# Optimization experiments

Measured on AMD Instinct MI355X. Metric: run time of the kernel, lower is better.

Reference implementation:

```python
import jax, jax.numpy as jnp
import numpy as np

N = 4096
NFEAT = 1024
NHID = 512
NCLS = 32
NLAYERS = 3
SPARSITY = 0.002


def _l2norm(x, eps=1e-12):
    n = jnp.sqrt(jnp.sum(x * x, axis=1, keepdims=True))
    return x / jnp.maximum(n, eps)


def setup_inputs() -> dict:
    key = jax.random.key(0)
    ks = jax.random.split(key, 12)
    # sparse-valued dense adjacency (original stores torch.sparse but densifies every hop)
    vals = jax.random.uniform(ks[0], (N, N), dtype=jnp.float32)
    mask = jax.random.uniform(ks[1], (N, N)) < SPARSITY
    adj = jnp.where(mask, vals, 0.0)
    features = jax.random.normal(ks[2], (N, NFEAT), dtype=jnp.float32)
    # y is a one-hot label matrix [N, nclass]
    labels = jax.random.randint(ks[3], (N,), 0, NCLS)
    y = jax.nn.one_hot(labels, NCLS, dtype=jnp.float32)
    s = 0.02
    W0 = jax.random.normal(ks[4], (NFEAT + 3 * NCLS, NHID), dtype=jnp.float32) * s
    b0 = jnp.zeros((NHID,), jnp.float32)
    W1_0 = jax.random.normal(ks[5], (NHID + 3 * NCLS, NHID), dtype=jnp.float32) * s
    b1_0 = jnp.zeros((NHID,), jnp.float32)
    W1_1 = jax.random.normal(ks[6], (NHID + 3 * NCLS, NHID), dtype=jnp.float32) * s
    b1_1 = jnp.zeros((NHID,), jnp.float32)
    W2 = jax.random.normal(ks[7], (NFEAT + NHID, NCLS), dtype=jnp.float32) * s
    b2 = jnp.zeros((NCLS,), jnp.float32)
    alphas = jnp.ones((NLAYERS, 5), jnp.float32)
    return {
        "adj": adj, "features": features, "y": y,
        "W0": W0, "b0": b0, "W1_0": W1_0, "b1_0": b1_0,
        "W1_1": W1_1, "b1_1": b1_1, "W2": W2, "b2": b2,
        "alphas": alphas, "layer_norm": 1,
    }


def reference(adj, features, y, W0, b0, W1_0, b1_0, W1_1, b1_1, W2, b2, alphas, layer_norm):
    Ws = [(W0, b0), (W1_0, b1_0), (W1_1, b1_1)]
    initial_features = jax.lax.stop_gradient(features)  # .clone().detach()
    feats = features
    max_features = None
    pow_adj = adj  # persists across layers (faithful to original): hops adj, adj^2, adj^4
    for i in range(NLAYERS):
        mask_alpha = jax.nn.softmax(alphas[i], axis=0)
        for _ in range(i):
            pow_adj = adj @ pow_adj
        hop = pow_adj @ feats                                   # [N, d]
        dist = (pow_adj > 0).astype(adj.dtype)                  # binarized reachability
        y_out = dist @ y                                        # [N, c]
        y_in = dist.T @ y                                       # [N, c]
        y_all = y_in + y_out
        hop = mask_alpha[0] * hop
        y_out = mask_alpha[1] * y_out
        y_in = mask_alpha[2] * y_in
        y_all = mask_alpha[3] * y_all
        mat = jnp.concatenate([hop, y_out, y_in, y_all], axis=1)
        W, b = Ws[i]
        tmp = mat @ W + b
        if layer_norm:
            tmp = _l2norm(tmp)
        feats = tmp
        max_features = tmp if max_features is None else jnp.maximum(max_features, tmp)
    final_mat = jnp.concatenate([initial_features, max_features], axis=1)
    out = jax.nn.relu(final_mat)
    # dropout: eval mode (identity)
    out = out @ W2 + b2
    return jax.nn.log_softmax(out, axis=1)
```

## Files before the change

### kernel.cpp

```cpp
#include <hip/hip_runtime.h>
#include <hip/hip_bf16.h>
#include <math.h>

typedef unsigned long long u64;
typedef unsigned short ushort_t;
typedef float f32x4 __attribute__((ext_vector_type(4)));
typedef short s16x8 __attribute__((ext_vector_type(8)));

#define NN 4096
#define NF 1024
#define NH 512
#define NC 32
#define LDP 40
#define K0 (NF + 3*NC)
#define K1 (NH + 3*NC)

__device__ inline float bf2f(ushort_t u) {
    unsigned int v = ((unsigned int)u) << 16;
    return __uint_as_float(v);
}
__device__ inline ushort_t f2bf(float f) {
    __hip_bfloat16 h = __float2bfloat16(f);
    return *(ushort_t*)&h;
}

__device__ void role_build(int i, int l, const float* __restrict__ adj,
                           u64* __restrict__ B1, int* __restrict__ rowcnt,
                           int* __restrict__ colidx, float* __restrict__ vals) {
    const float* row = adj + (size_t)i * NN + l * 64;
    const float4* row4 = (const float4*)row;
    u64 w = 0;
    #pragma unroll
    for (int k = 0; k < 16; ++k) {
        float4 v = row4[k];
        if (v.x > 0.f) w |= 1ULL << (4*k + 0);
        if (v.y > 0.f) w |= 1ULL << (4*k + 1);
        if (v.z > 0.f) w |= 1ULL << (4*k + 2);
        if (v.w > 0.f) w |= 1ULL << (4*k + 3);
    }
    B1[(size_t)i*64 + l] = w;
    int cnt = __popcll(w);
    int pre = cnt;
    #pragma unroll
    for (int o = 1; o < 64; o <<= 1) {
        int u = __shfl_up(pre, o, 64);
        if (l >= o) pre += u;
    }
    int excl = pre - cnt;
    int total = __shfl(pre, 63, 64);
    u64 ww = w;
    int idx = excl;
    while (ww) {
        int b = __ffsll((unsigned long long)ww) - 1;
        ww &= ww - 1;
        if (idx < 64) {
            colidx[i*64 + idx] = l*64 + b;
            vals[i*64 + idx] = row[b];
        }
        ++idx;
    }
    int tot = total < 64 ? total : 64;
    for (int s = tot + l; s < 64; s += 64) {
        colidx[i*64 + s] = 0;
        vals[i*64 + s] = 0.f;
    }
    if (l == 0) rowcnt[i] = (tot + 3) & ~3;
}

__global__ __launch_bounds__(256) void k_setup(const float* __restrict__ adj,
        const float* __restrict__ features, __hip_bfloat16* __restrict__ featb,
        const float* __restrict__ y, u64* __restrict__ LC,
        const float* __restrict__ W0, const float* __restrict__ W1_0,
        const float* __restrict__ W1_1,
        __hip_bfloat16* __restrict__ Wt0, __hip_bfloat16* __restrict__ Wt1,
        __hip_bfloat16* __restrict__ Wt2,
        const float* __restrict__ alphas, float* __restrict__ a_sm,
        u64* __restrict__ B1, int* __restrict__ rowcnt,
        int* __restrict__ colidx, float* __restrict__ vals) {
    __shared__ __align__(16) char smem[4352];
    int b = blockIdx.x;
    int t = threadIdx.x;
    int wid = t >> 6, l = t & 63;
    if (b < 1024) {
        role_build(b*4 + wid, l, adj, B1, rowcnt, colidx, vals);
    } else if (b < 5120) {
        int base = (b - 1024) * 1024 + t * 4;
        float4 v = *(const float4*)&features[base];
        ushort4 o;
        o.x = f2bf(v.x); o.y = f2bf(v.y); o.z = f2bf(v.z); o.w = f2bf(v.w);
        *(ushort4*)&((ushort_t*)featb)[base] = o;
    } else if (b < 5136) {
        int w = (b - 5120) * 4 + wid;
        const float* yr = y + (size_t)(w*64 + l) * NC;
        for (int c = 0; c < NC; ++c) {
            u64 m = __ballot(yr[c] > 0.5f);
            if (l == c) LC[c*64 + w] = m;
        }
    } else if (b < 6304) {
        const float* W; __hip_bfloat16* Wt; int K, ktiles, idx;
        if (b < 5696)      { W = W0;   Wt = Wt0; K = K0; ktiles = 35; idx = b - 5136; }
        else if (b < 6000) { W = W1_0; Wt = Wt1; K = K1; ktiles = 19; idx = b - 5696; }
        else               { W = W1_1; Wt = Wt2; K = K1; ktiles = 19; idx = b - 6000; }
        float (*tile)[33] = (float(*)[33])smem;
        int kb = (idx % ktiles) * 32, nb = (idx / ktiles) * 32;
        int tc = t & 31, tr8 = t >> 5;
        for (int r = tr8; r < 32; r += 8)
            tile[r][tc] = W[(size_t)(kb + r) * NH + nb + tc];
        __syncthreads();
        ushort_t* Wu = (ushort_t*)Wt;
        for (int r = tr8; r < 32; r += 8)
            Wu[(size_t)(nb + r) * K + kb + tc] = f2bf(tile[tc][r]);
    } else {
        if (t == 0) {
            for (int i = 0; i < 3; ++i) {
                float m = -1e30f;
                for (int j = 0; j < 5; ++j) m = fmaxf(m, alphas[i*5+j]);
                float e[5]; float s = 0.f;
                for (int j = 0; j < 5; ++j) { e[j] = expf(alphas[i*5+j] - m); s += e[j]; }
                for (int j = 0; j < 5; ++j) a_sm[i*5+j] = e[j] / s;
            }
        }
    }
}

__device__ void role_bsq(int i, int t, char* smem, const u64* __restrict__ Bidx,
                         const u64* __restrict__ Bdat, u64* __restrict__ Bout) {
    u64* ridx = (u64*)smem;
    u64* part = ridx + 64;
    int wid = t >> 6, lane = t & 63;
    if (t < 64) ridx[t] = Bidx[(size_t)i*64 + t];
    __syncthreads();
    u64 acc = 0;
    for (int u = wid*16; u < wid*16 + 16; ++u) {
        u64 w = ridx[u];
        while (w) {
            int k = u*64 + (__ffsll((unsigned long long)w) - 1);
            w &= (w - 1);
            acc |= Bdat[(size_t)k*64 + lane];
        }
    }
    part[wid*64 + lane] = acc;
    __syncthreads();
    if (t < 64) Bout[(size_t)i*64 + t] = part[t] | part[64+t] | part[128+t] | part[192+t];
}

__device__ void role_btrans(int tb, int wid, int l, char* smem,
                            const u64* __restrict__ B, u64* __restrict__ BT) {
    u64* ld = ((u64*)smem) + wid*64;
    int I = tb >> 6, J = tb & 63;
    ld[l] = B[(size_t)(I*64 + l)*64 + J];
    __syncthreads();
    u64 out = 0;
    #pragma unroll
    for (int r = 0; r < 64; ++r) out |= ((ld[r] >> l) & 1ULL) << r;
    BT[(size_t)(J*64 + l)*64 + I] = out;
}

__device__ void role_ymat(int rb, int t, char* smem, const u64* __restrict__ B,
                          const u64* __restrict__ BT, const u64* __restrict__ LC,
                          const float* __restrict__ asp, ushort_t* __restrict__ m,
                          int d, int K) {
    u64* LCt   = (u64*)smem;
    u64* rows  = LCt + 64*32;
    u64* rowsT = rows + 8*64;
    for (int k = t; k < 2048; k += 256) {
        int c = k >> 6, w = k & 63;
        LCt[w*32 + c] = LC[k];
    }
    for (int k = t; k < 512; k += 256) {
        int r = k >> 6, w = k & 63;
        rows[r*64 + w]  = B[(size_t)(rb + r)*64 + w];
        rowsT[r*64 + w] = BT[(size_t)(rb + r)*64 + w];
    }
    __syncthreads();
    int wid = t >> 6, lane = t & 63;
    int h = lane >> 5, c = lane & 31;
    int r = wid * 2 + h;
    int co = 0, ci = 0;
    #pragma unroll
    for (int w = 0; w < 64; ++w) {
        u64 lc = LCt[w*32 + c];
        co += __popcll(rows[r*64 + w]  & lc);
        ci += __popcll(rowsT[r*64 + w] & lc);
    }
    float a1 = asp[1], a2 = asp[2], a3 = asp[3];
    size_t i = rb + r;
    m[i*K + d + c]      = f2bf(a1 * (float)co);
    m[i*K + d + 32 + c] = f2bf(a2 * (float)ci);
    m[i*K + d + 64 + c] = f2bf(a3 * (float)(co + ci));
}

__device__ void role_spmm_bf(int i, int tx, const int* __restrict__ rc,
                             const int* __restrict__ ci, const float* __restrict__ vl,
                             const ushort_t* __restrict__ X, int d,
                             ushort_t* __restrict__ Y, int ystride, float alpha) {
    int cnt = rc[i];
    float acc[8] = {0,0,0,0,0,0,0,0};
    for (int p = 0; p < cnt; p += 4) {
        int4   cc = *(const int4*)&ci[(size_t)i*64 + p];
        float4 vv = *(const float4*)&vl[(size_t)i*64 + p];
        s16x8 x0 = *(const s16x8*)&X[(size_t)cc.x * d + 8*tx];
        s16x8 x1 = *(const s16x8*)&X[(size_t)cc.y * d + 8*tx];
        s16x8 x2 = *(const s16x8*)&X[(size_t)cc.z * d + 8*tx];
        s16x8 x3 = *(const s16x8*)&X[(size_t)cc.w * d + 8*tx];
        #pragma unroll
        for (int j = 0; j < 8; ++j) {
            acc[j] += vv.x * bf2f((ushort_t)x0[j]);
            acc[j] += vv.y * bf2f((ushort_t)x1[j]);
            acc[j] += vv.z * bf2f((ushort_t)x2[j]);
            acc[j] += vv.w * bf2f((ushort_t)x3[j]);
        }
    }
    s16x8 o;
    #pragma unroll
    for (int j = 0; j < 8; ++j) o[j] = (short)f2bf(alpha * acc[j]);
    *(s16x8*)&Y[(size_t)i*ystride + 8*tx] = o;
}

__device__ void role_spmm_f32s(int i, int tx, const int* __restrict__ rc,
                               const int* __restrict__ ci, const float* __restrict__ vl,
                               const float* __restrict__ src, const float* __restrict__ parts,
                               int ln, ushort_t* __restrict__ Y, int ystride, float alpha) {
    int cnt = rc[i];
    float acc[8] = {0,0,0,0,0,0,0,0};
    for (int p = 0; p < cnt; p += 4) {
        int4   cc = *(const int4*)&ci[(size_t)i*64 + p];
        float4 vv = *(const float4*)&vl[(size_t)i*64 + p];
        int cols[4] = {cc.x, cc.y, cc.z, cc.w};
        float vs4[4] = {vv.x, vv.y, vv.z, vv.w};
        #pragma unroll
        for (int e = 0; e < 4; ++e) {
            int col = cols[e];
            float4 pa = *(const float4*)&parts[col*8];
            float4 pb = *(const float4*)&parts[col*8 + 4];
            float ss = pa.x+pa.y+pa.z+pa.w + pb.x+pb.y+pb.z+pb.w;
            float sc = ln ? 1.0f / fmaxf(sqrtf(ss), 1e-12f) : 1.0f;
            float vsc = vs4[e] * sc;
            float4 xa = *(const float4*)&src[(size_t)col*NH + 8*tx];
            float4 xb = *(const float4*)&src[(size_t)col*NH + 8*tx + 4];
            acc[0] += vsc*xa.x; acc[1] += vsc*xa.y; acc[2] += vsc*xa.z; acc[3] += vsc*xa.w;
            acc[4] += vsc*xb.x; acc[5] += vsc*xb.y; acc[6] += vsc*xb.z; acc[7] += vsc*xb.w;
        }
    }
    s16x8 o;
    #pragma unroll
    for (int j = 0; j < 8; ++j) o[j] = (short)f2bf(alpha * acc[j]);
    *(s16x8*)&Y[(size_t)i*ystride + 8*tx] = o;
}

__device__ void role_gemm(int bx, int tid, char* smem,
                          const ushort_t* __restrict__ mat, const ushort_t* __restrict__ Wt,
                          const float* __restrict__ bias, float* __restrict__ C,
                          float* __restrict__ parts, int K) {
    ushort_t* As = (ushort_t*)smem;
    ushort_t* Bs = As + 64*LDP;
    int xcd = bx & 7, rest = bx >> 3;
    int nt = rest & 7, mt = (rest >> 3) * 8 + xcd;
    int bm = mt * 64, bn = nt * 64;
    int srow = tid >> 2, scol = (tid & 3) * 8;
    int wid = tid >> 6, lane = tid & 63;
    int fr = lane & 15, hi2 = lane >> 4, fk = hi2 * 8;
    f32x4 acc[4] = {{0,0,0,0},{0,0,0,0},{0,0,0,0},{0,0,0,0}};
    const ushort_t* Au = mat + (size_t)(bm + srow) * K + scol;
    const ushort_t* Bu = Wt  + (size_t)(bn + srow) * K + scol;
    for (int k0 = 0; k0 < K; k0 += 32) {
        *(s16x8*)&As[srow * LDP + scol] = *(const s16x8*)(Au + k0);
        *(s16x8*)&Bs[srow * LDP + scol] = *(const s16x8*)(Bu + k0);
        __syncthreads();
        s16x8 af = *(const s16x8*)&As[(wid * 16 + fr) * LDP + fk];
        #pragma unroll
        for (int j = 0; j < 4; ++j) {
            s16x8 bfv = *(const s16x8*)&Bs[(j * 16 + fr) * LDP + fk];
            acc[j] = __builtin_amdgcn_mfma_f32_16x16x32_bf16(af, bfv, acc[j], 0, 0, 0);
        }
        __syncthreads();
    }
    int drow = bm + wid * 16 + hi2 * 4;
    #pragma unroll
    for (int r = 0; r < 4; ++r) {
        float ps = 0.f;
        #pragma unroll
        for (int j = 0; j < 4; ++j) {
            float v = acc[j][r] + bias[bn + j*16 + fr];
            ps += v * v;
        }
        #pragma unroll
        for (int o = 1; o < 16; o <<= 1) ps += __shfl_xor(ps, o, 64);
        if (fr == 0) parts[(size_t)(drow + r) * 8 + nt] = ps;
    }
    #pragma unroll
    for (int j = 0; j < 4; ++j) {
        int col = bn + j * 16 + fr;
        float bv = bias[col];
        #pragma unroll
        for (int r = 0; r < 4; ++r)
            C[(size_t)(drow + r) * NH + col] = acc[j][r] + bv;
    }
}

__global__ __launch_bounds__(256) void k_phase2(const int* __restrict__ rowcnt,
        const int* __restrict__ colidx, const float* __restrict__ vals,
        const __hip_bfloat16* __restrict__ featb, __hip_bfloat16* __restrict__ mat0,
        const float* __restrict__ a_sm,
        const u64* __restrict__ B1, u64* __restrict__ B2, u64* __restrict__ B1T) {
    __shared__ __align__(16) char smem[2560];
    int b = blockIdx.x;
    int t = threadIdx.x;
    int wid = t >> 6, l = t & 63;
    if (b < 2048) {
        role_spmm_bf(b*2 + (t >> 7), t & 127, rowcnt, colidx, vals,
                     (const ushort_t*)featb, NF, (ushort_t*)mat0, K0, a_sm[0]);
    } else if (b < 6144) {
        role_bsq(b - 2048, t, smem, B1, B1, B2);
    } else {
        role_btrans((b - 6144)*4 + wid, wid, l, smem, B1, B1T);
    }
}

__global__ __launch_bounds__(256) void k_phase3(const u64* __restrict__ B1,
        const u64* __restrict__ B2, u64* __restrict__ B3, u64* __restrict__ B2T,
        const u64* __restrict__ B1T, const u64* __restrict__ LC,
        const float* __restrict__ a_sm, __hip_bfloat16* __restrict__ mat0) {
    __shared__ __align__(16) char smem[24576];
    int b = blockIdx.x;
    int t = threadIdx.x;
    int wid = t >> 6, l = t & 63;
    if (b < 4096) {
        role_bsq(b, t, smem, B1, B2, B3);
    } else if (b < 5120) {
        role_btrans((b - 4096)*4 + wid, wid, l, smem, B2, B2T);
    } else {
        role_ymat((b - 5120)*8, t, smem, B1, B1T, LC, a_sm, (ushort_t*)mat0, NF, K0);
    }
}

__global__ __launch_bounds__(256) void k_phase4(const __hip_bfloat16* __restrict__ mat0,
        const __hip_bfloat16* __restrict__ Wt0, const float* __restrict__ b0,
        float* __restrict__ tmp0, float* __restrict__ parts0,
        const u64* __restrict__ B1, const u64* __restrict__ B3, u64* __restrict__ B4,
        const u64* __restrict__ B2, const u64* __restrict__ B2T,
        const u64* __restrict__ LC, const float* __restrict__ a_sm,
        __hip_bfloat16* __restrict__ mat1) {
    __shared__ __align__(16) char smem[24576];
    int b = blockIdx.x;
    int t = threadIdx.x;
    if (b < 512) {
        role_gemm(b, t, smem, (const ushort_t*)mat0, (const ushort_t*)Wt0, b0,
                  tmp0, parts0, K0);
    } else if (b < 4608) {
        role_bsq(b - 512, t, smem, B1, B3, B4);
    } else {
        role_ymat((b - 4608)*8, t, smem, B2, B2T, LC, a_sm + 5, (ushort_t*)mat1, NH, K1);
    }
}

__global__ __launch_bounds__(256) void k_phase5(const u64* __restrict__ B4,
        u64* __restrict__ B4T,
        const int* __restrict__ rowcnt, const int* __restrict__ colidx,
        const float* __restrict__ vals, const float* __restrict__ tmp0,
        const float* __restrict__ parts0, const int* __restrict__ lnflag,
        __hip_bfloat16* __restrict__ u1) {
    __shared__ __align__(16) char smem[2048];
    int b = blockIdx.x;
    int t = threadIdx.x;
    int wid = t >> 6, l = t & 63;
    if (b < 1024) {
        role_btrans(b*4 + wid, wid, l, smem, B4, B4T);
    } else {
        role_spmm_f32s((b - 1024)*4 + wid, l, rowcnt, colidx, vals, tmp0, parts0,
                       *lnflag, (ushort_t*)u1, NH, 1.0f);
    }
}

__global__ __launch_bounds__(256) void k_phase6(const int* __restrict__ rowcnt,
        const int* __restrict__ colidx, const float* __restrict__ vals,
        const __hip_bfloat16* __restrict__ u1, __hip_bfloat16* __restrict__ mat1,
        const float* __restrict__ a_sm,
        const u64* __restrict__ B4, const u64* __restrict__ B4T,
        const u64* __restrict__ LC, __hip_bfloat16* __restrict__ mat2) {
    __shared__ __align__(16) char smem[24576];
    int b = blockIdx.x;
    int t = threadIdx.x;
    if (b < 1024) {
        role_spmm_bf(b*4 + (t >> 6), t & 63, rowcnt, colidx, vals,
                     (const ushort_t*)u1, NH, (ushort_t*)mat1, K1, a_sm[5]);
    } else {
        role_ymat((b - 1024)*8, t, smem, B4, B4T, LC, a_sm + 10, (ushort_t*)mat2, NH, K1);
    }
}

__global__ __launch_bounds__(256) void k_gemm(const __hip_bfloat16* __restrict__ mat,
        const __hip_bfloat16* __restrict__ Wt, const float* __restrict__ bias,
        float* __restrict__ C, float* __restrict__ parts, int K) {
    __shared__ __align__(16) char smem[2 * 64 * LDP * 2];
    role_gemm(blockIdx.x, threadIdx.x, smem, (const ushort_t*)mat, (const ushort_t*)Wt,
              bias, C, parts, K);
}

__global__ __launch_bounds__(256) void k_spmm_f(const int* __restrict__ rc,
        const int* __restrict__ ci, const float* __restrict__ vl,
        const float* __restrict__ src, const float* __restrict__ parts,
        const int* __restrict__ lnflag, __hip_bfloat16* __restrict__ Y,
        int ystride) {
    role_spmm_f32s(blockIdx.x*4 + (threadIdx.x >> 6), threadIdx.x & 63, rc, ci, vl,
                   src, parts, *lnflag, (ushort_t*)Y, ystride, 1.0f);
}

__global__ __launch_bounds__(256) void k_spmm_b(const int* __restrict__ rc,
        const int* __restrict__ ci, const float* __restrict__ vl,
        const __hip_bfloat16* __restrict__ X, __hip_bfloat16* __restrict__ Y,
        int ystride, const float* __restrict__ a_sm, int ai) {
    float alpha = (ai >= 0) ? a_sm[ai] : 1.0f;
    role_spmm_bf(blockIdx.x*4 + (threadIdx.x >> 6), threadIdx.x & 63, rc, ci, vl,
                 (const ushort_t*)X, NH, (ushort_t*)Y, ystride, alpha);
}

__global__ __launch_bounds__(256) void k_l2final(const float* __restrict__ tmp0,
        const float* __restrict__ parts0, const float* __restrict__ tmp1,
        const float* __restrict__ parts1, const float* __restrict__ tmp2,
        const float* __restrict__ parts2, const float* __restrict__ feat0,
        const float* __restrict__ W2, const float* __restrict__ b2,
        const int* __restrict__ lnflag, float* __restrict__ out) {
    int rb = blockIdx.x * 8;
    int t = threadIdx.x;
    __shared__ float rows[8][NF + NH];
    __shared__ float part[8][8][32];
    for (int r = 0; r < 8; ++r) {
        const float* f0 = feat0 + (size_t)(rb + r) * NF;
        for (int c = t; c < NF; c += 256) rows[r][c] = fmaxf(f0[c], 0.f);
    }
    int wid = t >> 6, lane = t & 63;
    int ln = *lnflag;
    #pragma unroll
    for (int rr = 0; rr < 2; ++rr) {
        int r = wid * 2 + rr;
        int row = rb + r;
        float s0, s1, s2;
        {
            float4 a0 = *(const float4*)&parts0[row*8], b0v = *(const float4*)&parts0[row*8+4];
            float4 a1 = *(const float4*)&parts1[row*8], b1v = *(const float4*)&parts1[row*8+4];
            float4 a2 = *(const float4*)&parts2[row*8], b2v = *(const float4*)&parts2[row*8+4];
            float q0 = a0.x+a0.y+a0.z+a0.w + b0v.x+b0v.y+b0v.z+b0v.w;
            float q1 = a1.x+a1.y+a1.z+a1.w + b1v.x+b1v.y+b1v.z+b1v.w;
            float q2 = a2.x+a2.y+a2.z+a2.w + b2v.x+b2v.y+b2v.z+b2v.w;
            s0 = ln ? 1.0f / fmaxf(sqrtf(q0), 1e-12f) : 1.0f;
            s1 = ln ? 1.0f / fmaxf(sqrtf(q1), 1e-12f) : 1.0f;
            s2 = ln ? 1.0f / fmaxf(sqrtf(q2), 1e-12f) : 1.0f;
        }
        const float4* t0 = (const float4*)(tmp0 + (size_t)row * NH + lane * 8);
        const float4* t1 = (const float4*)(tmp1 + (size_t)row * NH + lane * 8);
        const float4* t2 = (const float4*)(tmp2 + (size_t)row * NH + lane * 8);
        float* dst = &rows[r][NF + lane * 8];
        #pragma unroll
        for (int h = 0; h < 2; ++h) {
            float4 v0 = t0[h], v1 = t1[h], v2 = t2[h];
            dst[h*4+0] = fmaxf(fmaxf(fmaxf(v0.x*s0, v1.x*s1), v2.x*s2), 0.f);
            dst[h*4+1] = fmaxf(fmaxf(fmaxf(v0.y*s0, v1.y*s1), v2.y*s2), 0.f);
            dst[h*4+2] = fmaxf(fmaxf(fmaxf(v0.z*s0, v1.z*s1), v2.z*s2), 0.f);
            dst[h*4+3] = fmaxf(fmaxf(fmaxf(v0.w*s0, v1.w*s1), v2.w*s2), 0.f);
        }
    }
    __syncthreads();
    int c = t & 31, g = t >> 5;
    float acc[8] = {0,0,0,0,0,0,0,0};
    for (int k = g * 192; k < (g + 1) * 192; ++k) {
        float w = W2[(size_t)k * NC + c];
        #pragma unroll
        for (int r = 0; r < 8; ++r) acc[r] += rows[r][k] * w;
    }
    #pragma unroll
    for (int r = 0; r < 8; ++r) part[g][r][c] = acc[r];
    __syncthreads();
    int r = g;
    float lg = b2[c];
    #pragma unroll
    for (int gg = 0; gg < 8; ++gg) lg += part[gg][r][c];
    float m = lg;
    #pragma unroll
    for (int o = 16; o > 0; o >>= 1) m = fmaxf(m, __shfl_xor(m, o, 32));
    float e = expf(lg - m), s = e;
    #pragma unroll
    for (int o = 16; o > 0; o >>= 1) s += __shfl_xor(s, o, 32);
    out[(size_t)(rb + r) * NC + c] = lg - m - logf(s);
}

extern "C" void kernel_launch(void* const* d_in, const int* in_sizes, int n_in,
                              void* d_out, int out_size, void* d_ws, size_t ws_size,
                              hipStream_t stream) {
    const float* adj      = (const float*)d_in[0];
    const float* features = (const float*)d_in[1];
    const float* y        = (const float*)d_in[2];
    const float* W0       = (const float*)d_in[3];
    const float* b0       = (const float*)d_in[4];
    const float* W1_0     = (const float*)d_in[5];
    const float* b1_0     = (const float*)d_in[6];
    const float* W1_1     = (const float*)d_in[7];
    const float* b1_1     = (const float*)d_in[8];
    const float* W2       = (const float*)d_in[9];
    const float* b2       = (const float*)d_in[10];
    const float* alphas   = (const float*)d_in[11];
    const int*   lnflag   = (const int*)d_in[12];
    float* out = (float*)d_out;

    char* ws = (char*)d_ws;
    size_t off = 0;
    auto alloc = [&](size_t bytes) -> char* {
        char* p = ws + off;
        off = (off + bytes + 255) & ~(size_t)255;
        return p;
    };
    float* a_sm   = (float*)alloc(16 * 4);
    int*   rowcnt = (int*)alloc((size_t)NN * 4);
    int*   colidx = (int*)alloc((size_t)NN * 64 * 4);
    float* vals   = (float*)alloc((size_t)NN * 64 * 4);
    u64* B1  = (u64*)alloc((size_t)NN * 64 * 8);
    u64* B2  = (u64*)alloc((size_t)NN * 64 * 8);
    u64* B3  = (u64*)alloc((size_t)NN * 64 * 8);
    u64* B4  = (u64*)alloc((size_t)NN * 64 * 8);
    u64* B1T = (u64*)alloc((size_t)NN * 64 * 8);
    u64* B2T = (u64*)alloc((size_t)NN * 64 * 8);
    u64* B4T = (u64*)alloc((size_t)NN * 64 * 8);
    u64* LC  = (u64*)alloc((size_t)NC * 64 * 8);
    __hip_bfloat16* featb = (__hip_bfloat16*)alloc((size_t)NN * NF * 2);
    __hip_bfloat16* t1b   = (__hip_bfloat16*)alloc((size_t)NN * NH * 2);
    __hip_bfloat16* t2b   = (__hip_bfloat16*)alloc((size_t)NN * NH * 2);
    __hip_bfloat16* mat0  = (__hip_bfloat16*)alloc((size_t)NN * K0 * 2);
    __hip_bfloat16* mat1  = (__hip_bfloat16*)alloc((size_t)NN * K1 * 2);
    __hip_bfloat16* mat2  = (__hip_bfloat16*)alloc((size_t)NN * K1 * 2);
    __hip_bfloat16* Wt0   = (__hip_bfloat16*)alloc((size_t)NH * K0 * 2);
    __hip_bfloat16* Wt1   = (__hip_bfloat16*)alloc((size_t)NH * K1 * 2);
    __hip_bfloat16* Wt2   = (__hip_bfloat16*)alloc((size_t)NH * K1 * 2);
    float* tmp0   = (float*)alloc((size_t)NN * NH * 4);
    float* tmp1   = (float*)alloc((size_t)NN * NH * 4);
    float* tmp2   = (float*)alloc((size_t)NN * NH * 4);
    float* parts0 = (float*)alloc((size_t)NN * 8 * 4);
    float* parts1 = (float*)alloc((size_t)NN * 8 * 4);
    float* parts2 = (float*)alloc((size_t)NN * 8 * 4);

    k_setup<<<6305, 256, 0, stream>>>(adj, features, featb, y, LC, W0, W1_0, W1_1,
                                      Wt0, Wt1, Wt2, alphas, a_sm,
                                      B1, rowcnt, colidx, vals);
    k_phase2<<<7168, 256, 0, stream>>>(rowcnt, colidx, vals, featb, mat0, a_sm,
                                       B1, B2, B1T);
    k_phase3<<<5632, 256, 0, stream>>>(B1, B2, B3, B2T, B1T, LC, a_sm, mat0);
    k_phase4<<<5120, 256, 0, stream>>>(mat0, Wt0, b0, tmp0, parts0,
                                       B1, B3, B4, B2, B2T, LC, a_sm, mat1);
    k_phase5<<<2048, 256, 0, stream>>>(B4, B4T, rowcnt, colidx, vals,
                                       tmp0, parts0, lnflag, t1b);
    k_phase6<<<1536, 256, 0, stream>>>(rowcnt, colidx, vals, t1b, mat1, a_sm,
                                       B4, B4T, LC, mat2);
    k_gemm<<<512, 256, 0, stream>>>(mat1, Wt1, b1_0, tmp1, parts1, K1);
    k_spmm_f<<<NN/4, 256, 0, stream>>>(rowcnt, colidx, vals, tmp1, parts1, lnflag, t1b, NH);
    k_spmm_b<<<NN/4, 256, 0, stream>>>(rowcnt, colidx, vals, t1b, t2b, NH, a_sm, -1);
    k_spmm_b<<<NN/4, 256, 0, stream>>>(rowcnt, colidx, vals, t2b, t1b, NH, a_sm, -1);
    k_spmm_b<<<NN/4, 256, 0, stream>>>(rowcnt, colidx, vals, t1b, mat2, K1, a_sm, 10);
    k_gemm<<<512, 256, 0, stream>>>(mat2, Wt2, b1_1, tmp2, parts2, K1);
    k_l2final<<<NN/8, 256, 0, stream>>>(tmp0, parts0, tmp1, parts1, tmp2, parts2,
                                        features, W2, b2, lnflag, out);
}
```

Before: 215.5 us.

## Reassociate hops: multiply features by weights before sparse propagation, split label-count GEMM

After: 236.8 us. 9.9% more time.

```diff
diff --git a/kernel.cpp b/kernel.cpp
--- a/kernel.cpp
+++ b/kernel.cpp
@@ -12,8 +12,6 @@
 #define NH 512
 #define NC 32
 #define LDP 40
-#define K0 (NF + 3*NC)
-#define K1 (NH + 3*NC)
 
 __device__ inline float bf2f(ushort_t u) {
     unsigned int v = ((unsigned int)u) << 16;
@@ -64,63 +62,23 @@
         colidx[i*64 + s] = 0;
         vals[i*64 + s] = 0.f;
     }
-    if (l == 0) rowcnt[i] = (tot + 3) & ~3;
-}
-
-__global__ __launch_bounds__(256) void k_setup(const float* __restrict__ adj,
-        const float* __restrict__ features, __hip_bfloat16* __restrict__ featb,
-        const float* __restrict__ y, u64* __restrict__ LC,
-        const float* __restrict__ W0, const float* __restrict__ W1_0,
-        const float* __restrict__ W1_1,
-        __hip_bfloat16* __restrict__ Wt0, __hip_bfloat16* __restrict__ Wt1,
-        __hip_bfloat16* __restrict__ Wt2,
-        const float* __restrict__ alphas, float* __restrict__ a_sm,
-        u64* __restrict__ B1, int* __restrict__ rowcnt,
-        int* __restrict__ colidx, float* __restrict__ vals) {
-    __shared__ __align__(16) char smem[4352];
-    int b = blockIdx.x;
-    int t = threadIdx.x;
-    int wid = t >> 6, l = t & 63;
-    if (b < 1024) {
-        role_build(b*4 + wid, l, adj, B1, rowcnt, colidx, vals);
-    } else if (b < 5120) {
-        int base = (b - 1024) * 1024 + t * 4;
-        float4 v = *(const float4*)&features[base];
-        ushort4 o;
-        o.x = f2bf(v.x); o.y = f2bf(v.y); o.z = f2bf(v.z); o.w = f2bf(v.w);
-        *(ushort4*)&((ushort_t*)featb)[base] = o;
-    } else if (b < 5136) {
-        int w = (b - 5120) * 4 + wid;
-        const float* yr = y + (size_t)(w*64 + l) * NC;
-        for (int c = 0; c < NC; ++c) {
-            u64 m = __ballot(yr[c] > 0.5f);
-            if (l == c) LC[c*64 + w] = m;
-        }
-    } else if (b < 6304) {
-        const float* W; __hip_bfloat16* Wt; int K, ktiles, idx;
-        if (b < 5696)      { W = W0;   Wt = Wt0; K = K0; ktiles = 35; idx = b - 5136; }
-        else if (b < 6000) { W = W1_0; Wt = Wt1; K = K1; ktiles = 19; idx = b - 5696; }
-        else               { W = W1_1; Wt = Wt2; K = K1; ktiles = 19; idx = b - 6000; }
-        float (*tile)[33] = (float(*)[33])smem;
-        int kb = (idx % ktiles) * 32, nb = (idx / ktiles) * 32;
-        int tc = t & 31, tr8 = t >> 5;
-        for (int r = tr8; r < 32; r += 8)
-            tile[r][tc] = W[(size_t)(kb + r) * NH + nb + tc];
-        __syncthreads();
-        ushort_t* Wu = (ushort_t*)Wt;
-        for (int r = tr8; r < 32; r += 8)
-            Wu[(size_t)(nb + r) * K + kb + tc] = f2bf(tile[tc][r]);
-    } else {
-        if (t == 0) {
-            for (int i = 0; i < 3; ++i) {
-                float m = -1e30f;
-                for (int j = 0; j < 5; ++j) m = fmaxf(m, alphas[i*5+j]);
-                float e[5]; float s = 0.f;
-                for (int j = 0; j < 5; ++j) { e[j] = expf(alphas[i*5+j] - m); s += e[j]; }
-                for (int j = 0; j < 5; ++j) a_sm[i*5+j] = e[j] / s;
-            }
-        }
-    }
+    if (l == 0) {
+        int r8 = (tot + 7) & ~7;
+        rowcnt[i] = r8 < 64 ? r8 : 64;
+    }
+}
+
+__device__ void role_wt(const float* __restrict__ W, ushort_t* __restrict__ Wt,
+                        int ksrc0, int Kd, int idx, char* smem, int t) {
+    float (*tile)[33] = (float(*)[33])smem;
+    int ktiles = Kd >> 5;
+    int kb = (idx % ktiles) * 32, nb = (idx / ktiles) * 32;
+    int tc = t & 31, tr8 = t >> 5;
+    for (int r = tr8; r < 32; r += 8)
+        tile[r][tc] = W[(size_t)(ksrc0 + kb + r) * NH + nb + tc];
+    __syncthreads();
+    for (int r = tr8; r < 32; r += 8)
+        Wt[(size_t)(nb + r) * Kd + kb + tc] = f2bf(tile[tc][r]);
 }
 
 __device__ void role_bsq(int i, int t, char* smem, const u64* __restrict__ Bidx,
@@ -158,8 +116,7 @@
 
 __device__ void role_ymat(int rb, int t, char* smem, const u64* __restrict__ B,
                           const u64* __restrict__ BT, const u64* __restrict__ LC,
-                          const float* __restrict__ asp, ushort_t* __restrict__ m,
-                          int d, int K) {
+                          const float* __restrict__ asp, ushort_t* __restrict__ yc) {
     u64* LCt   = (u64*)smem;
     u64* rows  = LCt + 64*32;
     u64* rowsT = rows + 8*64;
@@ -185,73 +142,15 @@
     }
     float a1 = asp[1], a2 = asp[2], a3 = asp[3];
     size_t i = rb + r;
-    m[i*K + d + c]      = f2bf(a1 * (float)co);
-    m[i*K + d + 32 + c] = f2bf(a2 * (float)ci);
-    m[i*K + d + 64 + c] = f2bf(a3 * (float)(co + ci));
-}
-
-__device__ void role_spmm_bf(int i, int tx, const int* __restrict__ rc,
-                             const int* __restrict__ ci, const float* __restrict__ vl,
-                             const ushort_t* __restrict__ X, int d,
-                             ushort_t* __restrict__ Y, int ystride, float alpha) {
-    int cnt = rc[i];
-    float acc[8] = {0,0,0,0,0,0,0,0};
-    for (int p = 0; p < cnt; p += 4) {
-        int4   cc = *(const int4*)&ci[(size_t)i*64 + p];
-        float4 vv = *(const float4*)&vl[(size_t)i*64 + p];
-        s16x8 x0 = *(const s16x8*)&X[(size_t)cc.x * d + 8*tx];
-        s16x8 x1 = *(const s16x8*)&X[(size_t)cc.y * d + 8*tx];
-        s16x8 x2 = *(const s16x8*)&X[(size_t)cc.z * d + 8*tx];
-        s16x8 x3 = *(const s16x8*)&X[(size_t)cc.w * d + 8*tx];
-        #pragma unroll
-        for (int j = 0; j < 8; ++j) {
-            acc[j] += vv.x * bf2f((ushort_t)x0[j]);
-            acc[j] += vv.y * bf2f((ushort_t)x1[j]);
-            acc[j] += vv.z * bf2f((ushort_t)x2[j]);
-            acc[j] += vv.w * bf2f((ushort_t)x3[j]);
-        }
-    }
-    s16x8 o;
-    #pragma unroll
-    for (int j = 0; j < 8; ++j) o[j] = (short)f2bf(alpha * acc[j]);
-    *(s16x8*)&Y[(size_t)i*ystride + 8*tx] = o;
-}
-
-__device__ void role_spmm_f32s(int i, int tx, const int* __restrict__ rc,
-                               const int* __restrict__ ci, const float* __restrict__ vl,
-                               const float* __restrict__ src, const float* __restrict__ parts,
-                               int ln, ushort_t* __restrict__ Y, int ystride, float alpha) {
-    int cnt = rc[i];
-    float acc[8] = {0,0,0,0,0,0,0,0};
-    for (int p = 0; p < cnt; p += 4) {
-        int4   cc = *(const int4*)&ci[(size_t)i*64 + p];
-        float4 vv = *(const float4*)&vl[(size_t)i*64 + p];
-        int cols[4] = {cc.x, cc.y, cc.z, cc.w};
-        float vs4[4] = {vv.x, vv.y, vv.z, vv.w};
-        #pragma unroll
-        for (int e = 0; e < 4; ++e) {
-            int col = cols[e];
-            float4 pa = *(const float4*)&parts[col*8];
-            float4 pb = *(const float4*)&parts[col*8 + 4];
-            float ss = pa.x+pa.y+pa.z+pa.w + pb.x+pb.y+pb.z+pb.w;
-            float sc = ln ? 1.0f / fmaxf(sqrtf(ss), 1e-12f) : 1.0f;
-            float vsc = vs4[e] * sc;
-            float4 xa = *(const float4*)&src[(size_t)col*NH + 8*tx];
-            float4 xb = *(const float4*)&src[(size_t)col*NH + 8*tx + 4];
-            acc[0] += vsc*xa.x; acc[1] += vsc*xa.y; acc[2] += vsc*xa.z; acc[3] += vsc*xa.w;
-            acc[4] += vsc*xb.x; acc[5] += vsc*xb.y; acc[6] += vsc*xb.z; acc[7] += vsc*xb.w;
-        }
-    }
-    s16x8 o;
-    #pragma unroll
-    for (int j = 0; j < 8; ++j) o[j] = (short)f2bf(alpha * acc[j]);
-    *(s16x8*)&Y[(size_t)i*ystride + 8*tx] = o;
-}
-
-__device__ void role_gemm(int bx, int tid, char* smem,
-                          const ushort_t* __restrict__ mat, const ushort_t* __restrict__ Wt,
-                          const float* __restrict__ bias, float* __restrict__ C,
-                          float* __restrict__ parts, int K) {
+    yc[i*96 + c]      = f2bf(a1 * (float)co);
+    yc[i*96 + 32 + c] = f2bf(a2 * (float)ci);
+    yc[i*96 + 64 + c] = f2bf(a3 * (float)(co + ci));
+}
+
+__device__ void role_gemm(int bx, int tid, char* smem, const ushort_t* __restrict__ Abf,
+                          const float* __restrict__ Af, int Ka,
+                          const ushort_t* __restrict__ Bt, int K,
+                          ushort_t* __restrict__ Cb, float* __restrict__ Cf) {
     ushort_t* As = (ushort_t*)smem;
     ushort_t* Bs = As + 64*LDP;
     int xcd = bx & 7, rest = bx >> 3;
@@ -261,11 +160,23 @@
     int wid = tid >> 6, lane = tid & 63;
     int fr = lane & 15, hi2 = lane >> 4, fk = hi2 * 8;
     f32x4 acc[4] = {{0,0,0,0},{0,0,0,0},{0,0,0,0},{0,0,0,0}};
-    const ushort_t* Au = mat + (size_t)(bm + srow) * K + scol;
-    const ushort_t* Bu = Wt  + (size_t)(bn + srow) * K + scol;
     for (int k0 = 0; k0 < K; k0 += 32) {
-        *(s16x8*)&As[srow * LDP + scol] = *(const s16x8*)(Au + k0);
-        *(s16x8*)&Bs[srow * LDP + scol] = *(const s16x8*)(Bu + k0);
+        if (Abf) {
+            *(s16x8*)&As[srow * LDP + scol] =
+                *(const s16x8*)&Abf[(size_t)(bm + srow) * Ka + k0 + scol];
+        } else {
+            const float* ap = &Af[(size_t)(bm + srow) * Ka + k0 + scol];
+            float4 a0 = *(const float4*)ap;
+            float4 a1 = *(const float4*)(ap + 4);
+            s16x8 o;
+            o[0] = (short)f2bf(a0.x); o[1] = (short)f2bf(a0.y);
+            o[2] = (short)f2bf(a0.z); o[3] = (short)f2bf(a0.w);
+            o[4] = (short)f2bf(a1.x); o[5] = (short)f2bf(a1.y);
+            o[6] = (short)f2bf(a1.z); o[7] = (short)f2bf(a1.w);
+            *(s16x8*)&As[srow * LDP + scol] = o;
+        }
+        *(s16x8*)&Bs[srow * LDP + scol] =
+            *(const s16x8*)&Bt[(size_t)(bn + srow) * K + k0 + scol];
         __syncthreads();
         s16x8 af = *(const s16x8*)&As[(wid * 16 + fr) * LDP + fk];
         #pragma unroll
@@ -277,211 +188,303 @@
     }
     int drow = bm + wid * 16 + hi2 * 4;
     #pragma unroll
-    for (int r = 0; r < 4; ++r) {
-        float ps = 0.f;
-        #pragma unroll
-        for (int j = 0; j < 4; ++j) {
-            float v = acc[j][r] + bias[bn + j*16 + fr];
-            ps += v * v;
-        }
-        #pragma unroll
-        for (int o = 1; o < 16; o <<= 1) ps += __shfl_xor(ps, o, 64);
-        if (fr == 0) parts[(size_t)(drow + r) * 8 + nt] = ps;
-    }
-    #pragma unroll
     for (int j = 0; j < 4; ++j) {
         int col = bn + j * 16 + fr;
-        float bv = bias[col];
         #pragma unroll
-        for (int r = 0; r < 4; ++r)
-            C[(size_t)(drow + r) * NH + col] = acc[j][r] + bv;
-    }
-}
-
-__global__ __launch_bounds__(256) void k_phase2(const int* __restrict__ rowcnt,
-        const int* __restrict__ colidx, const float* __restrict__ vals,
-        const __hip_bfloat16* __restrict__ featb, __hip_bfloat16* __restrict__ mat0,
-        const float* __restrict__ a_sm,
-        const u64* __restrict__ B1, u64* __restrict__ B2, u64* __restrict__ B1T) {
-    __shared__ __align__(16) char smem[2560];
-    int b = blockIdx.x;
-    int t = threadIdx.x;
+        for (int r = 0; r < 4; ++r) {
+            if (Cb) Cb[(size_t)(drow + r) * NH + col] = f2bf(acc[j][r]);
+            else    Cf[(size_t)(drow + r) * NH + col] = acc[j][r];
+        }
+    }
+}
+
+__device__ void role_sfin(int blk, int t, const float* __restrict__ F,
+                          const float* __restrict__ W2, float* __restrict__ sl) {
+    int r = t >> 5, c = t & 31;
+    int row = blk * 8 + r;
+    const float* fr_ = F + (size_t)row * NF;
+    float acc = 0.f;
+    for (int k = 0; k < NF; k += 4) {
+        float4 fv = *(const float4*)&fr_[k];
+        acc += fmaxf(fv.x, 0.f) * W2[(size_t)(k+0)*NC + c];
+        acc += fmaxf(fv.y, 0.f) * W2[(size_t)(k+1)*NC + c];
+        acc += fmaxf(fv.z, 0.f) * W2[(size_t)(k+2)*NC + c];
+        acc += fmaxf(fv.w, 0.f) * W2[(size_t)(k+3)*NC + c];
+    }
+    sl[(size_t)row*NC + c] = acc;
+}
+
+__device__ void role_spmm(int i, int lane, const int* __restrict__ rc,
+                          const int* __restrict__ ci, const float* __restrict__ vl,
+                          const ushort_t* __restrict__ X, ushort_t* __restrict__ Y) {
+    int cnt = rc[i];
+    float acc[8] = {0,0,0,0,0,0,0,0};
+    for (int p = 0; p < cnt; p += 8) {
+        int4   c0 = *(const int4*)&ci[i*64 + p];
+        int4   c1 = *(const int4*)&ci[i*64 + p + 4];
+        float4 v0 = *(const float4*)&vl[i*64 + p];
+        float4 v1 = *(const float4*)&vl[i*64 + p + 4];
+        s16x8 x0 = *(const s16x8*)&X[(size_t)c0.x * NH + 8*lane];
+        s16x8 x1 = *(const s16x8*)&X[(size_t)c0.y * NH + 8*lane];
+        s16x8 x2 = *(const s16x8*)&X[(size_t)c0.z * NH + 8*lane];
+        s16x8 x3 = *(const s16x8*)&X[(size_t)c0.w * NH + 8*lane];
+        s16x8 x4 = *(const s16x8*)&X[(size_t)c1.x * NH + 8*lane];
+        s16x8 x5 = *(const s16x8*)&X[(size_t)c1.y * NH + 8*lane];
+        s16x8 x6 = *(const s16x8*)&X[(size_t)c1.z * NH + 8*lane];
+        s16x8 x7 = *(const s16x8*)&X[(size_t)c1.w * NH + 8*lane];
+        #pragma unroll
+        for (int j = 0; j < 8; ++j) {
+            acc[j] += v0.x * bf2f((ushort_t)x0[j]);
+            acc[j] += v0.y * bf2f((ushort_t)x1[j]);
+            acc[j] += v0.z * bf2f((ushort_t)x2[j]);
+            acc[j] += v0.w * bf2f((ushort_t)x3[j]);
+            acc[j] += v1.x * bf2f((ushort_t)x4[j]);
+            acc[j] += v1.y * bf2f((ushort_t)x5[j]);
+            acc[j] += v1.z * bf2f((ushort_t)x6[j]);
+            acc[j] += v1.w * bf2f((ushort_t)x7[j]);
+        }
+    }
+    s16x8 o;
+    #pragma unroll
+    for (int j = 0; j < 8; ++j) o[j] = (short)f2bf(acc[j]);
+    *(s16x8*)&Y[(size_t)i*NH + 8*lane] = o;
+}
+
+__device__ void role_spmmF(int i, int lane, const int* __restrict__ rc,
+                           const int* __restrict__ ci, const float* __restrict__ vl,
+                           const ushort_t* __restrict__ X, const float* __restrict__ yv,
+                           const float* __restrict__ bias, int ln, float alpha,
+                           ushort_t* __restrict__ F) {
+    int cnt = rc[i];
+    float acc[8] = {0,0,0,0,0,0,0,0};
+    for (int p = 0; p < cnt; p += 8) {
+        int4   c0 = *(const int4*)&ci[i*64 + p];
+        int4   c1 = *(const int4*)&ci[i*64 + p + 4];
+        float4 v0 = *(const float4*)&vl[i*64 + p];
+        float4 v1 = *(const float4*)&vl[i*64 + p + 4];
+        s16x8 x0 = *(const s16x8*)&X[(size_t)c0.x * NH + 8*lane];
+        s16x8 x1 = *(const s16x8*)&X[(size_t)c0.y * NH + 8*lane];
+        s16x8 x2 = *(const s16x8*)&X[(size_t)c0.z * NH + 8*lane];
+        s16x8 x3 = *(const s16x8*)&X[(size_t)c0.w * NH + 8*lane];
+        s16x8 x4 = *(const s16x8*)&X[(size_t)c1.x * NH + 8*lane];
+        s16x8 x5 = *(const s16x8*)&X[(size_t)c1.y * NH + 8*lane];
+        s16x8 x6 = *(const s16x8*)&X[(size_t)c1.z * NH + 8*lane];
+        s16x8 x7 = *(const s16x8*)&X[(size_t)c1.w * NH + 8*lane];
+        #pragma unroll
+        for (int j = 0; j < 8; ++j) {
+            acc[j] += v0.x * bf2f((ushort_t)x0[j]);
+            acc[j] += v0.y * bf2f((ushort_t)x1[j]);
+            acc[j] += v0.z * bf2f((ushort_t)x2[j]);
+            acc[j] += v0.w * bf2f((ushort_t)x3[j]);
+            acc[j] += v1.x * bf2f((ushort_t)x4[j]);
+            acc[j] += v1.y * bf2f((ushort_t)x5[j]);
+            acc[j] += v1.z * bf2f((ushort_t)x6[j]);
+            acc[j] += v1.w * bf2f((ushort_t)x7[j]);
+        }
+    }
+    const float* yr = yv + (size_t)i * NH + 8*lane;
+    float4 ya = *(const float4*)yr;
+    float4 yb = *(const float4*)(yr + 4);
+    float4 ba = *(const float4*)&bias[8*lane];
+    float4 bb = *(const float4*)&bias[8*lane + 4];
+    float v[8];
+    v[0] = alpha*acc[0] + ya.x + ba.x; v[1] = alpha*acc[1] + ya.y + ba.y;
+    v[2] = alpha*acc[2] + ya.z + ba.z; v[3] = alpha*acc[3] + ya.w + ba.w;
+    v[4] = alpha*acc[4] + yb.x + bb.x; v[5] = alpha*acc[5] + yb.y + bb.y;
+    v[6] = alpha*acc[6] + yb.z + bb.z; v[7] = alpha*acc[7] + yb.w + bb.w;
+    float ss = 0.f;
+    #pragma unroll
+    for (int j = 0; j < 8; ++j) ss += v[j]*v[j];
+    #pragma unroll
+    for (int o = 1; o < 64; o <<= 1) ss += __shfl_xor(ss, o, 64);
+    float sc = ln ? 1.0f / fmaxf(sqrtf(ss), 1e-12f) : 1.0f;
+    s16x8 o;
+    #pragma unroll
+    for (int j = 0; j < 8; ++j) o[j] = (short)f2bf(v[j] * sc);
+    *(s16x8*)&F[(size_t)i*NH + 8*lane] = o;
+}
+
+__global__ __launch_bounds__(256) void k_setup(const float* __restrict__ adj,
+        const float* __restrict__ y, u64* __restrict__ LC,
+        const float* __restrict__ W0, const float* __restrict__ W1_0,
+        const float* __restrict__ W1_1,
+        ushort_t* __restrict__ Wh0t, ushort_t* __restrict__ Wy0t,
+        ushort_t* __restrict__ Wh1t, ushort_t* __restrict__ Wy1t,
+        ushort_t* __restrict__ Wh2t, ushort_t* __restrict__ Wy2t,
+        const float* __restrict__ alphas, float* __restrict__ a_sm,
+        u64* __restrict__ B1, int* __restrict__ rowcnt,
+        int* __restrict__ colidx, float* __restrict__ vals) {
+    __shared__ __align__(16) char smem[4352];
+    int b = blockIdx.x, t = threadIdx.x;
     int wid = t >> 6, l = t & 63;
-    if (b < 2048) {
-        role_spmm_bf(b*2 + (t >> 7), t & 127, rowcnt, colidx, vals,
-                     (const ushort_t*)featb, NF, (ushort_t*)mat0, K0, a_sm[0]);
-    } else if (b < 6144) {
-        role_bsq(b - 2048, t, smem, B1, B1, B2);
-    } else {
-        role_btrans((b - 6144)*4 + wid, wid, l, smem, B1, B1T);
-    }
-}
-
-__global__ __launch_bounds__(256) void k_phase3(const u64* __restrict__ B1,
+    if (b < 1024) {
+        role_build(b*4 + wid, l, adj, B1, rowcnt, colidx, vals);
+    } else if (b < 1040) {
+        int w = (b - 1024) * 4 + wid;
+        const float* yr = y + (size_t)(w*64 + l) * NC;
+        for (int c = 0; c < NC; ++c) {
+            u64 m = __ballot(yr[c] > 0.5f);
+            if (l == c) LC[c*64 + w] = m;
+        }
+    } else if (b < 1552) { role_wt(W0,   Wh0t, 0,    NF, b - 1040, smem, t); }
+    else if (b < 1600)   { role_wt(W0,   Wy0t, NF,   96, b - 1552, smem, t); }
+    else if (b < 1856)   { role_wt(W1_0, Wh1t, 0,    NH, b - 1600, smem, t); }
+    else if (b < 1904)   { role_wt(W1_0, Wy1t, NH,   96, b - 1856, smem, t); }
+    else if (b < 2160)   { role_wt(W1_1, Wh2t, 0,    NH, b - 1904, smem, t); }
+    else if (b < 2208)   { role_wt(W1_1, Wy2t, NH,   96, b - 2160, smem, t); }
+    else {
+        if (t == 0) {
+            for (int i = 0; i < 3; ++i) {
+                float m = -1e30f;
+                for (int j = 0; j < 5; ++j) m = fmaxf(m, alphas[i*5+j]);
+                float e[5]; float s = 0.f;
+                for (int j = 0; j < 5; ++j) { e[j] = expf(alphas[i*5+j] - m); s += e[j]; }
+                for (int j = 0; j < 5; ++j) a_sm[i*5+j] = e[j] / s;
+            }
+        }
+    }
+}
+
+__global__ __launch_bounds__(256) void k_p2(const float* __restrict__ features,
+        const ushort_t* __restrict__ Wh0t, ushort_t* __restrict__ zb,
+        const u64* __restrict__ B1, u64* __restrict__ B2, u64* __restrict__ B1T,
+        const float* __restrict__ W2, float* __restrict__ sl) {
+    __shared__ __align__(16) char smem[10240];
+    int b = blockIdx.x, t = threadIdx.x;
+    int wid = t >> 6, l = t & 63;
+    if (b < 512)       role_gemm(b, t, smem, nullptr, features, NF, Wh0t, NF, zb, nullptr);
+    else if (b < 4608) role_bsq(b - 512, t, smem, B1, B1, B2);
+    else if (b < 5632) role_btrans((b - 4608)*4 + wid, wid, l, smem, B1, B1T);
+    else               role_sfin(b - 5632, t, features, W2, sl);
+}
+
+__global__ __launch_bounds__(256) void k_p3(const u64* __restrict__ B1,
         const u64* __restrict__ B2, u64* __restrict__ B3, u64* __restrict__ B2T,
         const u64* __restrict__ B1T, const u64* __restrict__ LC,
-        const float* __restrict__ a_sm, __hip_bfloat16* __restrict__ mat0) {
+        const float* __restrict__ a_sm, ushort_t* __restrict__ y0c) {
     __shared__ __align__(16) char smem[24576];
-    int b = blockIdx.x;
-    int t = threadIdx.x;
+    int b = blockIdx.x, t = threadIdx.x;
     int wid = t >> 6, l = t & 63;
-    if (b < 4096) {
-        role_bsq(b, t, smem, B1, B2, B3);
-    } else if (b < 5120) {
-        role_btrans((b - 4096)*4 + wid, wid, l, smem, B2, B2T);
-    } else {
-        role_ymat((b - 5120)*8, t, smem, B1, B1T, LC, a_sm, (ushort_t*)mat0, NF, K0);
-    }
-}
-
-__global__ __launch_bounds__(256) void k_phase4(const __hip_bfloat16* __restrict__ mat0,
-        const __hip_bfloat16* __restrict__ Wt0, const float* __restrict__ b0,
-        float* __restrict__ tmp0, float* __restrict__ parts0,
-        const u64* __restrict__ B1, const u64* __restrict__ B3, u64* __restrict__ B4,
+    if (b < 4096)      role_bsq(b, t, smem, B1, B2, B3);
+    else if (b < 5120) role_btrans((b - 4096)*4 + wid, wid, l, smem, B2, B2T);
+    else               role_ymat((b - 5120)*8, t, smem, B1, B1T, LC, a_sm, y0c);
+}
+
+__global__ __launch_bounds__(256) void k_p4(const ushort_t* __restrict__ y0c,
+        const ushort_t* __restrict__ Wy0t, float* __restrict__ yv0,
         const u64* __restrict__ B2, const u64* __restrict__ B2T,
         const u64* __restrict__ LC, const float* __restrict__ a_sm,
-        __hip_bfloat16* __restrict__ mat1) {
+        ushort_t* __restrict__ y1c,
+        const u64* __restrict__ B1, const u64* __restrict__ B3, u64* __restrict__ B4) {
     __shared__ __align__(16) char smem[24576];
-    int b = blockIdx.x;
-    int t = threadIdx.x;
-    if (b < 512) {
-        role_gemm(b, t, smem, (const ushort_t*)mat0, (const ushort_t*)Wt0, b0,
-                  tmp0, parts0, K0);
-    } else if (b < 4608) {
-        role_bsq(b - 512, t, smem, B1, B3, B4);
-    } else {
-        role_ymat((b - 4608)*8, t, smem, B2, B2T, LC, a_sm + 5, (ushort_t*)mat1, NH, K1);
-    }
-}
-
-__global__ __launch_bounds__(256) void k_phase5(const u64* __restrict__ B4,
-        u64* __restrict__ B4T,
-        const int* __restrict__ rowcnt, const int* __restrict__ colidx,
-        const float* __restrict__ vals, const float* __restrict__ tmp0,
-        const float* __restrict__ parts0, const int* __restrict__ lnflag,
-        __hip_bfloat16* __restrict__ u1) {
-    __shared__ __align__(16) char smem[2048];
-    int b = blockIdx.x;
-    int t = threadIdx.x;
+    int b = blockIdx.x, t = threadIdx.x;
+    if (b < 512)       role_gemm(b, t, smem, y0c, nullptr, 96, Wy0t, 96, nullptr, yv0);
+    else if (b < 1024) role_ymat((b - 512)*8, t, smem, B2, B2T, LC, a_sm + 5, y1c);
+    else               role_bsq(b - 1024, t, smem, B1, B3, B4);
+}
+
+__global__ __launch_bounds__(256) void k_p5(const int* __restrict__ rc,
+        const int* __restrict__ ci, const float* __restrict__ vl,
+        const ushort_t* __restrict__ zb, const float* __restrict__ yv0,
+        const float* __restrict__ b0, const int* __restrict__ lnflag,
+        const float* __restrict__ a_sm, ushort_t* __restrict__ f1,
+        const u64* __restrict__ B4, u64* __restrict__ B4T,
+        const ushort_t* __restrict__ y1c, const ushort_t* __restrict__ Wy1t,
+        float* __restrict__ yv1) {
+    __shared__ __align__(16) char smem[10240];
+    int b = blockIdx.x, t = threadIdx.x;
     int wid = t >> 6, l = t & 63;
-    if (b < 1024) {
-        role_btrans(b*4 + wid, wid, l, smem, B4, B4T);
-    } else {
-        role_spmm_f32s((b - 1024)*4 + wid, l, rowcnt, colidx, vals, tmp0, parts0,
-                       *lnflag, (ushort_t*)u1, NH, 1.0f);
-    }
-}
-
-__global__ __launch_bounds__(256) void k_phase6(const int* __restrict__ rowcnt,
-        const int* __restrict__ colidx, const float* __restrict__ vals,
-        const __hip_bfloat16* __restrict__ u1, __hip_bfloat16* __restrict__ mat1,
-        const float* __restrict__ a_sm,
+    if (b < 1024)
+        role_spmmF(b*4 + wid, l, rc, ci, vl, zb, yv0, b0, *lnflag, a_sm[0], f1);
+    else if (b < 2048)
+        role_btrans((b - 1024)*4 + wid, wid, l, smem, B4, B4T);
+    else
+        role_gemm(b - 2048, t, smem, y1c, nullptr, 96, Wy1t, 96, nullptr, yv1);
+}
+
+__global__ __launch_bounds__(256) void k_p6(const ushort_t* __restrict__ f1,
+        const ushort_t* __restrict__ Wh1t, ushort_t* __restrict__ zb,
         const u64* __restrict__ B4, const u64* __restrict__ B4T,
-        const u64* __restrict__ LC, __hip_bfloat16* __restrict__ mat2) {
+        const u64* __restrict__ LC, const float* __restrict__ a_sm,
+        ushort_t* __restrict__ y2c) {
     __shared__ __align__(16) char smem[24576];
-    int b = blockIdx.x;
-    int t = threadIdx.x;
-    if (b < 1024) {
-        role_spmm_bf(b*4 + (t >> 6), t & 63, rowcnt, colidx, vals,
-                     (const ushort_t*)u1, NH, (ushort_t*)mat1, K1, a_sm[5]);
-    } else {
-        role_ymat((b - 1024)*8, t, smem, B4, B4T, LC, a_sm + 10, (ushort_t*)mat2, NH, K1);
-    }
-}
-
-__global__ __launch_bounds__(256) void k_gemm(const __hip_bfloat16* __restrict__ mat,
-        const __hip_bfloat16* __restrict__ Wt, const float* __restrict__ bias,
-        float* __restrict__ C, float* __restrict__ parts, int K) {
-    __shared__ __align__(16) char smem[2 * 64 * LDP * 2];
-    role_gemm(blockIdx.x, threadIdx.x, smem, (const ushort_t*)mat, (const ushort_t*)Wt,
-              bias, C, parts, K);
-}
-
-__global__ __launch_bounds__(256) void k_spmm_f(const int* __restrict__ rc,
+    int b = blockIdx.x, t = threadIdx.x;
+    if (b < 512) role_gemm(b, t, smem, f1, nullptr, NH, Wh1t, NH, zb, nullptr);
+    else         role_ymat((b - 512)*8, t, smem, B4, B4T, LC, a_sm + 10, y2c);
+}
+
+__global__ __launch_bounds__(256) void k_p7(const int* __restrict__ rc,
         const int* __restrict__ ci, const float* __restrict__ vl,
-        const float* __restrict__ src, const float* __restrict__ parts,
-        const int* __restrict__ lnflag, __hip_bfloat16* __restrict__ Y,
-        int ystride) {
-    role_spmm_f32s(blockIdx.x*4 + (threadIdx.x >> 6), threadIdx.x & 63, rc, ci, vl,
-                   src, parts, *lnflag, (ushort_t*)Y, ystride, 1.0f);
-}
-
-__global__ __launch_bounds__(256) void k_spmm_b(const int* __restrict__ rc,
+        const ushort_t* __restrict__ zb, ushort_t* __restrict__ ub,
+        const ushort_t* __restrict__ y2c, const ushort_t* __restrict__ Wy2t,
+        float* __restrict__ yv2) {
+    __shared__ __align__(16) char smem[10240];
+    int b = blockIdx.x, t = threadIdx.x;
+    int wid = t >> 6, l = t & 63;
+    if (b < 1024) role_spmm(b*4 + wid, l, rc, ci, vl, zb, ub);
+    else          role_gemm(b - 1024, t, smem, y2c, nullptr, 96, Wy2t, 96, nullptr, yv2);
+}
+
+__global__ __launch_bounds__(256) void k_spmm(const int* __restrict__ rc,
         const int* __restrict__ ci, const float* __restrict__ vl,
-        const __hip_bfloat16* __restrict__ X, __hip_bfloat16* __restrict__ Y,
-        int ystride, const float* __restrict__ a_sm, int ai) {
-    float alpha = (ai >= 0) ? a_sm[ai] : 1.0f;
-    role_spmm_bf(blockIdx.x*4 + (threadIdx.x >> 6), threadIdx.x & 63, rc, ci, vl,
-                 (const ushort_t*)X, NH, (ushort_t*)Y, ystride, alpha);
-}
-
-__global__ __launch_bounds__(256) void k_l2final(const float* __restrict__ tmp0,
-        const float* __restrict__ parts0, const float* __restrict__ tmp1,
-        const float* __restrict__ parts1, const float* __restrict__ tmp2,
-        const float* __restrict__ parts2, const float* __restrict__ feat0,
-        const float* __restrict__ W2, const float* __restrict__ b2,
-        const int* __restrict__ lnflag, float* __restrict__ out) {
-    int rb = blockIdx.x * 8;
-    int t = threadIdx.x;
-    __shared__ float rows[8][NF + NH];
-    __shared__ float part[8][8][32];
-    for (int r = 0; r < 8; ++r) {
-        const float* f0 = feat0 + (size_t)(rb + r) * NF;
-        for (int c = t; c < NF; c += 256) rows[r][c] = fmaxf(f0[c], 0.f);
-    }
-    int wid = t >> 6, lane = t & 63;
-    int ln = *lnflag;
-    #pragma unroll
-    for (int rr = 0; rr < 2; ++rr) {
-        int r = wid * 2 + rr;
-        int row = rb + r;
-        float s0, s1, s2;
-        {
-            float4 a0 = *(const float4*)&parts0[row*8], b0v = *(const float4*)&parts0[row*8+4];
-            float4 a1 = *(const float4*)&parts1[row*8], b1v = *(const float4*)&parts1[row*8+4];
-            float4 a2 = *(const float4*)&parts2[row*8], b2v = *(const float4*)&parts2[row*8+4];
-            float q0 = a0.x+a0.y+a0.z+a0.w + b0v.x+b0v.y+b0v.z+b0v.w;
-            float q1 = a1.x+a1.y+a1.z+a1.w + b1v.x+b1v.y+b1v.z+b1v.w;
-            float q2 = a2.x+a2.y+a2.z+a2.w + b2v.x+b2v.y+b2v.z+b2v.w;
-            s0 = ln ? 1.0f / fmaxf(sqrtf(q0), 1e-12f) : 1.0f;
-            s1 = ln ? 1.0f / fmaxf(sqrtf(q1), 1e-12f) : 1.0f;
-            s2 = ln ? 1.0f / fmaxf(sqrtf(q2), 1e-12f) : 1.0f;
-        }
-        const float4* t0 = (const float4*)(tmp0 + (size_t)row * NH + lane * 8);
-        const float4* t1 = (const float4*)(tmp1 + (size_t)row * NH + lane * 8);
-        const float4* t2 = (const float4*)(tmp2 + (size_t)row * NH + lane * 8);
-        float* dst = &rows[r][NF + lane * 8];
+        const ushort_t* __restrict__ X, ushort_t* __restrict__ Y) {
+    role_spmm(blockIdx.x*4 + (threadIdx.x >> 6), threadIdx.x & 63, rc, ci, vl, X, Y);
+}
+
+__global__ __launch_bounds__(256) void k_spmmF(const int* __restrict__ rc,
+        const int* __restrict__ ci, const float* __restrict__ vl,
+        const ushort_t* __restrict__ X, const float* __restrict__ yv,
+        const float* __restrict__ bias, const int* __restrict__ lnflag,
+        const float* __restrict__ a_sm, int ai, ushort_t* __restrict__ F) {
+    role_spmmF(blockIdx.x*4 + (threadIdx.x >> 6), threadIdx.x & 63, rc, ci, vl,
+               X, yv, bias, *lnflag, a_sm[ai], F);
+}
+
+__global__ __launch_bounds__(256) void k_gemmz(const ushort_t* __restrict__ A,
+        const ushort_t* __restrict__ Bt, ushort_t* __restrict__ C, int K) {
+    __shared__ __align__(16) char smem[10240];
+    role_gemm(blockIdx.x, threadIdx.x, smem, A, nullptr, K, Bt, K, C, nullptr);
+}
+
+__global__ __launch_bounds__(256) void k_final(const ushort_t* __restrict__ f1,
+        const ushort_t* __restrict__ f2, const ushort_t* __restrict__ f3,
+        const float* __restrict__ sl, const float* __restrict__ W2,
+        const float* __restrict__ b2, float* __restrict__ out) {
+    __shared__ float mrow[8][NH];
+    int blk = blockIdx.x, t = threadIdx.x;
+    int rb = blk * 8;
+    #pragma unroll
+    for (int q = 0; q < 2; ++q) {
+        int ch = t*2 + q;
+        int rr = ch >> 6, k8 = (ch & 63) * 8;
+        s16x8 a = *(const s16x8*)&f1[(size_t)(rb + rr)*NH + k8];
+        s16x8 bq = *(const s16x8*)&f2[(size_t)(rb + rr)*NH + k8];
+        s16x8 cq = *(const s16x8*)&f3[(size_t)(rb + rr)*NH + k8];
         #pragma unroll
-        for (int h = 0; h < 2; ++h) {
-            float4 v0 = t0[h], v1 = t1[h], v2 = t2[h];
-            dst[h*4+0] = fmaxf(fmaxf(fmaxf(v0.x*s0, v1.x*s1), v2.x*s2), 0.f);
-            dst[h*4+1] = fmaxf(fmaxf(fmaxf(v0.y*s0, v1.y*s1), v2.y*s2), 0.f);
-            dst[h*4+2] = fmaxf(fmaxf(fmaxf(v0.z*s0, v1.z*s1), v2.z*s2), 0.f);
-            dst[h*4+3] = fmaxf(fmaxf(fmaxf(v0.w*s0, v1.w*s1), v2.w*s2), 0.f);
+        for (int j = 0; j < 8; ++j) {
+            float m = fmaxf(fmaxf(bf2f((ushort_t)a[j]), bf2f((ushort_t)bq[j])),
+                            bf2f((ushort_t)cq[j]));
+            mrow[rr][k8 + j] = fmaxf(m, 0.f);
         }
     }
     __syncthreads();
-    int c = t & 31, g = t >> 5;
-    float acc[8] = {0,0,0,0,0,0,0,0};
-    for (int k = g * 192; k < (g + 1) * 192; ++k) {
-        float w = W2[(size_t)k * NC + c];
-        #pragma unroll
-        for (int r = 0; r < 8; ++r) acc[r] += rows[r][k] * w;
-    }
-    #pragma unroll
-    for (int r = 0; r < 8; ++r) part[g][r][c] = acc[r];
-    __syncthreads();
-    int r = g;
-    float lg = b2[c];
-    #pragma unroll
-    for (int gg = 0; gg < 8; ++gg) lg += part[gg][r][c];
-    float m = lg;
+    int r = t >> 5, c = t & 31;
+    int row = rb + r;
+    float acc = sl[(size_t)row*NC + c] + b2[c];
+    for (int k = 0; k < NH; k += 4) {
+        float4 mv = *(const float4*)&mrow[r][k];
+        acc += mv.x * W2[(size_t)(NF + k + 0)*NC + c];
+        acc += mv.y * W2[(size_t)(NF + k + 1)*NC + c];
+        acc += mv.z * W2[(size_t)(NF + k + 2)*NC + c];
+        acc += mv.w * W2[(size_t)(NF + k + 3)*NC + c];
+    }
+    float m = acc;
     #pragma unroll
     for (int o = 16; o > 0; o >>= 1) m = fmaxf(m, __shfl_xor(m, o, 32));
-    float e = expf(lg - m), s = e;
+    float e = expf(acc - m), s = e;
     #pragma unroll
     for (int o = 16; o > 0; o >>= 1) s += __shfl_xor(s, o, 32);
-    out[(size_t)(rb + r) * NC + c] = lg - m - logf(s);
+    out[(size_t)row*NC + c] = acc - m - logf(s);
 }
 
 extern "C" void kernel_launch(void* const* d_in, const int* in_sizes, int n_in,
@@ -521,40 +524,43 @@
     u64* B2T = (u64*)alloc((size_t)NN * 64 * 8);
     u64* B4T = (u64*)alloc((size_t)NN * 64 * 8);
     u64* LC  = (u64*)alloc((size_t)NC * 64 * 8);
-    __hip_bfloat16* featb = (__hip_bfloat16*)alloc((size_t)NN * NF * 2);
-    __hip_bfloat16* t1b   = (__hip_bfloat16*)alloc((size_t)NN * NH * 2);
-    __hip_bfloat16* t2b   = (__hip_bfloat16*)alloc((size_t)NN * NH * 2);
-    __hip_bfloat16* mat0  = (__hip_bfloat16*)alloc((size_t)NN * K0 * 2);
-    __hip_bfloat16* mat1  = (__hip_bfloat16*)alloc((size_t)NN * K1 * 2);
-    __hip_bfloat16* mat2  = (__hip_bfloat16*)alloc((size_t)NN * K1 * 2);
-    __hip_bfloat16* Wt0   = (__hip_bfloat16*)alloc((size_t)NH * K0 * 2);
-    __hip_bfloat16* Wt1   = (__hip_bfloat16*)alloc((size_t)NH * K1 * 2);
-    __hip_bfloat16* Wt2   = (__hip_bfloat16*)alloc((size_t)NH * K1 * 2);
-    float* tmp0   = (float*)alloc((size_t)NN * NH * 4);
-    float* tmp1   = (float*)alloc((size_t)NN * NH * 4);
-    float* tmp2   = (float*)alloc((size_t)NN * NH * 4);
-    float* parts0 = (float*)alloc((size_t)NN * 8 * 4);
-    float* parts1 = (float*)alloc((size_t)NN * 8 * 4);
-    float* parts2 = (float*)alloc((size_t)NN * 8 * 4);
-
-    k_setup<<<6305, 256, 0, stream>>>(adj, features, featb, y, LC, W0, W1_0, W1_1,
-                                      Wt0, Wt1, Wt2, alphas, a_sm,
-                                      B1, rowcnt, colidx, vals);
-    k_phase2<<<7168, 256, 0, stream>>>(rowcnt, colidx, vals, featb, mat0, a_sm,
-                                       B1, B2, B1T);
-    k_phase3<<<5632, 256, 0, stream>>>(B1, B2, B3, B2T, B1T, LC, a_sm, mat0);
-    k_phase4<<<5120, 256, 0, stream>>>(mat0, Wt0, b0, tmp0, parts0,
-                                       B1, B3, B4, B2, B2T, LC, a_sm, mat1);
-    k_phase5<<<2048, 256, 0, stream>>>(B4, B4T, rowcnt, colidx, vals,
-                                       tmp0, parts0, lnflag, t1b);
-    k_phase6<<<1536, 256, 0, stream>>>(rowcnt, colidx, vals, t1b, mat1, a_sm,
-                                       B4, B4T, LC, mat2);
-    k_gemm<<<512, 256, 0, stream>>>(mat1, Wt1, b1_0, tmp1, parts1, K1);
-    k_spmm_f<<<NN/4, 256, 0, stream>>>(rowcnt, colidx, vals, tmp1, parts1, lnflag, t1b, NH);
-    k_spmm_b<<<NN/4, 256, 0, stream>>>(rowcnt, colidx, vals, t1b, t2b, NH, a_sm, -1);
-    k_spmm_b<<<NN/4, 256, 0, stream>>>(rowcnt, colidx, vals, t2b, t1b, NH, a_sm, -1);
-    k_spmm_b<<<NN/4, 256, 0, stream>>>(rowcnt, colidx, vals, t1b, mat2, K1, a_sm, 10);
-    k_gemm<<<512, 256, 0, stream>>>(mat2, Wt2, b1_1, tmp2, parts2, K1);
-    k_l2final<<<NN/8, 256, 0, stream>>>(tmp0, parts0, tmp1, parts1, tmp2, parts2,
-                                        features, W2, b2, lnflag, out);
-}
+    ushort_t* Wh0t = (ushort_t*)alloc((size_t)NH * NF * 2);
+    ushort_t* Wh1t = (ushort_t*)alloc((size_t)NH * NH * 2);
+    ushort_t* Wh2t = (ushort_t*)alloc((size_t)NH * NH * 2);
+    ushort_t* Wy0t = (ushort_t*)alloc((size_t)NH * 96 * 2);
+    ushort_t* Wy1t = (ushort_t*)alloc((size_t)NH * 96 * 2);
+    ushort_t* Wy2t = (ushort_t*)alloc((size_t)NH * 96 * 2);
+    ushort_t* y0c  = (ushort_t*)alloc((size_t)NN * 96 * 2);
+    ushort_t* y1c  = (ushort_t*)alloc((size_t)NN * 96 * 2);
+    ushort_t* y2c  = (ushort_t*)alloc((size_t)NN * 96 * 2);
+    float* yv0 = (float*)alloc((size_t)NN * NH * 4);
+    float* yv1 = (float*)alloc((size_t)NN * NH * 4);
+    float* yv2 = (float*)alloc((size_t)NN * NH * 4);
+    ushort_t* zb = (ushort_t*)alloc((size_t)NN * NH * 2);
+    ushort_t* ub = (ushort_t*)alloc((size_t)NN * NH * 2);
+    ushort_t* vb = (ushort_t*)alloc((size_t)NN * NH * 2);
+    ushort_t* f1 = (ushort_t*)alloc((size_t)NN * NH * 2);
+    ushort_t* f2 = (ushort_t*)alloc((size_t)NN * NH * 2);
+    ushort_t* f3 = (ushort_t*)alloc((size_t)NN * NH * 2);
+    float* sl = (float*)alloc((size_t)NN * NC * 4);
+
+    k_setup<<<2209, 256, 0, stream>>>(adj, y, LC, W0, W1_0, W1_1,
+                                      Wh0t, Wy0t, Wh1t, Wy1t, Wh2t, Wy2t,
+                                      alphas, a_sm, B1, rowcnt, colidx, vals);
+    k_p2<<<6144, 256, 0, stream>>>(features, Wh0t, zb, B1, B2, B1T, W2, sl);
+    k_p3<<<5632, 256, 0, stream>>>(B1, B2, B3, B2T, B1T, LC, a_sm, y0c);
+    k_p4<<<5120, 256, 0, stream>>>(y0c, Wy0t, yv0, B2, B2T, LC, a_sm, y1c, B1, B3, B4);
+    k_p5<<<2560, 256, 0, stream>>>(rowcnt, colidx, vals, zb, yv0, b0, lnflag, a_sm,
+                                   f1, B4, B4T, y1c, Wy1t, yv1);
+    k_p6<<<1024, 256, 0, stream>>>(f1, Wh1t, zb, B4, B4T, LC, a_sm, y2c);
+    k_p7<<<1536, 256, 0, stream>>>(rowcnt, colidx, vals, zb, ub, y2c, Wy2t, yv2);
+    k_spmmF<<<1024, 256, 0, stream>>>(rowcnt, colidx, vals, ub, yv1, b1_0, lnflag,
+                                      a_sm, 5, f2);
+    k_gemmz<<<512, 256, 0, stream>>>(f2, Wh2t, zb, NH);
+    k_spmm<<<1024, 256, 0, stream>>>(rowcnt, colidx, vals, zb, ub);
+    k_spmm<<<1024, 256, 0, stream>>>(rowcnt, colidx, vals, ub, vb);
+    k_spmm<<<1024, 256, 0, stream>>>(rowcnt, colidx, vals, vb, ub);
+    k_spmmF<<<1024, 256, 0, stream>>>(rowcnt, colidx, vals, ub, yv2, b1_1, lnflag,
+                                      a_sm, 10, f3);
+    k_final<<<512, 256, 0, stream>>>(f1, f2, f3, sl, W2, b2, out);
+}
```
